# Kernel tuning notes

Measured on AMD Instinct MI355X. Metric: run time of the kernel, lower is better.

The kernel has to match this reference:

```python
import jax, jax.numpy as jnp
import numpy as np

B, C, H, W = 1, 128, 48, 48
HC = 32                     # head_channel
NH = C // HC                # num heads = 4
K = 16                      # n_clusters
N = H * W                   # 2304
SCALE = HC ** 0.5
EPS = 1e-6


def setup_inputs() -> dict:
    key = jax.random.key(0)
    ks = jax.random.split(key, 20)
    s = 0.05  # weight init scale ~ xavier-ish for C=128
    def g(i, shape, sc=s):
        return jax.random.normal(ks[i], shape, dtype=jnp.float32) * sc
    return {
        'q_img': g(0, (B, C, H, W), 1.0),
        'k_img_map': g(1, (B, C, H, W), 1.0),
        'v_img_map': g(2, (B, C, H, W), 1.0),
        'pixel_coefficients': jax.random.uniform(ks[3], (B, N, N), dtype=jnp.float32),
        'labels': jax.random.randint(ks[4], (B, H, W), 0, K),
        # projections (stored as [in, out]; y = x @ w + b)
        'wq': g(5, (C, C)), 'bq': jnp.zeros((C,), jnp.float32),
        'wk': g(6, (C, C)), 'bk': jnp.zeros((C,), jnp.float32),
        'wv': g(7, (C, C)), 'bv': jnp.zeros((C,), jnp.float32),
        # mlp_1: Linear(C,2C) -> LeakyReLU(0.01) -> Linear(2C,C) (dropout=0 -> identity)
        'w1a': g(8, (C, 2 * C)), 'b1a': jnp.zeros((2 * C,), jnp.float32),
        'w1b': g(9, (2 * C, C)), 'b1b': jnp.zeros((C,), jnp.float32),
        # mlp_2
        'w2a': g(10, (C, 2 * C)), 'b2a': jnp.zeros((2 * C,), jnp.float32),
        'w2b': g(11, (2 * C, C)), 'b2b': jnp.zeros((C,), jnp.float32),
    }


def _mlp(x, wa, ba, wb, bb):
    h = x @ wa + ba
    h = jax.nn.leaky_relu(h, negative_slope=0.01)
    return h @ wb + bb


def reference(q_img, k_img_map, v_img_map, pixel_coefficients,
              wq, bq, wk, bk, wv, bv,
              w1a, b1a, w1b, b1b, w2a, b2a, w2b, b2b,
              labels):
    # projections on channel-last pixels
    q = q_img.transpose(0, 2, 3, 1).reshape(B, N, C) @ wq + bq
    k = k_img_map.transpose(0, 2, 3, 1).reshape(B, N, C) @ wk + bk
    v = v_img_map.transpose(0, 2, 3, 1).reshape(B, N, C) @ wv + bv

    labels_flat = labels.reshape(B, N)
    onehot = jax.nn.one_hot(labels_flat, K, dtype=q.dtype)        # [B,N,K]
    num_k = jnp.einsum('bnk,bnc->bkc', onehot, k)                 # [B,K,C]
    den_k = onehot.sum(axis=1)[:, :, None] + EPS                  # [B,K,1]
    centers_k = num_k / den_k

    qm = q.reshape(B, N, NH, HC).transpose(0, 2, 1, 3)            # [B,h,N,d]
    km = k.reshape(B, N, NH, HC).transpose(0, 2, 1, 3)
    vm = v.reshape(B, N, NH, HC).transpose(0, 2, 1, 3)
    kcm = centers_k.reshape(B, K, NH, HC).transpose(0, 2, 1, 3)   # [B,h,K,d]

    attn_intra = jnp.einsum('bhid,bhjd->bhij', qm, km)            # [B,h,N,N]
    attn_centers = jnp.einsum('bhid,bhkd->bhik', qm, kcm)         # [B,h,N,K]

    # gather center score per key's cluster: attn_centers[b,h,i,labels[b,j]]
    idx = jnp.broadcast_to(labels_flat[:, None, None, :], (B, NH, N, N))
    attn_inter = jnp.take_along_axis(attn_centers, idx, axis=3)   # [B,h,N,N]
    attn_inter = attn_inter * pixel_coefficients[:, None, :, :]

    same = labels_flat[:, None, :, None] == labels_flat[:, None, None, :]  # [B,1,N,N]
    scores = jnp.where(same, attn_intra, attn_inter) / SCALE
    attn_w = jax.nn.softmax(scores, axis=-1)

    out = jnp.einsum('bhij,bhjd->bhid', attn_w, vm)
    out = out.transpose(0, 2, 1, 3).reshape(B, N, C)              # [B,N,C]

    v_spatial = v.reshape(B, H, W, C).transpose(0, 3, 1, 2)       # [B,C,H,W]
    rs1 = v_spatial + _mlp(out, w1a, b1a, w1b, b1b).transpose(0, 2, 1).reshape(B, C, H, W)
    rs1_flat = rs1.transpose(0, 2, 3, 1).reshape(B, N, C)
    rs2 = rs1 + _mlp(rs1_flat, w2a, b2a, w2b, b2b).transpose(0, 2, 1).reshape(B, C, H, W)
    return rs2
```

## Files before the change

### kernel.cpp

```cpp
#include <hip/hip_runtime.h>
#include <hip/hip_bf16.h>
#include <math.h>

#define NPIX 2304
#define CCH  128
#define NH   4
#define HC   32
#define NCL  16
#define KSPLIT 8
#define KEYS 288
#define NSTEP 9
#define QSCALE 0.25503489f
#define PPT  16

typedef __attribute__((ext_vector_type(8))) short short8;
typedef __attribute__((ext_vector_type(4))) short short4v;
typedef __attribute__((ext_vector_type(4))) float f32x4;

#if __has_builtin(__builtin_amdgcn_exp2f)
#define EXP2(x) __builtin_amdgcn_exp2f(x)
#else
#define EXP2(x) __expf((x) * 0.6931471805599453f)
#endif

static __device__ __forceinline__ short f2bf(float x) {
    __hip_bfloat16 b = __float2bfloat16(x);
    return *reinterpret_cast<short*>(&b);
}

__global__ void __launch_bounds__(256) proj_kernel(
        const float* __restrict__ xq, const float* __restrict__ xk,
        const float* __restrict__ xv, const int* __restrict__ labels,
        const float* __restrict__ wq, const float* __restrict__ bq,
        const float* __restrict__ wk, const float* __restrict__ bk,
        const float* __restrict__ wv, const float* __restrict__ bv,
        const float* __restrict__ w1a, const float* __restrict__ w1b,
        const float* __restrict__ w2a, const float* __restrict__ w2b,
        short* __restrict__ qbf, short* __restrict__ kbf,
        float* __restrict__ vbuf, short* __restrict__ vbfT,
        float* __restrict__ cpart, float* __restrict__ denpart,
        short* __restrict__ t1a, short* __restrict__ t1b,
        short* __restrict__ t2a, short* __restrict__ t2b) {
    __shared__ float xsP[CCH * PPT];
    __shared__ float ls2[2 * NCL * CCH];
    __shared__ float smls[32];
    const int which = blockIdx.y;
    const int pxblk = blockIdx.x;
    const int t  = threadIdx.x;

    if (which == 3) {
        const int idx = pxblk * 256 + t;
        if (idx < 16384) {
            const int sel = idx >> 12, local = idx & 4095;
            short8 s;
            if (sel == 0 || sel == 2) {
                const float* src = (sel == 0) ? w1a : w2a;
                short*       dst = (sel == 0) ? t1a : t2a;
                const int o = local >> 4, g = local & 15;
#pragma unroll
                for (int j = 0; j < 8; ++j) s[j] = f2bf(src[(g * 8 + j) * 256 + o]);
                *(short8*)(dst + (size_t)o * 128 + g * 8) = s;
            } else {
                const float* src = (sel == 1) ? w1b : w2b;
                short*       dst = (sel == 1) ? t1b : t2b;
                const int o = local >> 5, g = local & 31;
#pragma unroll
                for (int j = 0; j < 8; ++j) s[j] = f2bf(src[(g * 8 + j) * 128 + o]);
                *(short8*)(dst + (size_t)o * 256 + g * 8) = s;
            }
        }
        return;
    }

    const int n0 = pxblk * PPT;
    const int c  = t & 127;
    const int ph = t >> 7;
    const float* x = (which == 0) ? xq : (which == 1) ? xk : xv;
    const float* w = (which == 0) ? wq : (which == 1) ? wk : wv;
    const float* b = (which == 0) ? bq : (which == 1) ? bk : bv;

#pragma unroll
    for (int it = 0; it < 8; ++it) {
        const int flat = it * 256 + t;
        const int cc = flat >> 4;
        const int p  = flat & 15;
        xsP[flat] = x[cc * NPIX + n0 + p];
    }
    if (which == 1)
        for (int u = t; u < 2 * NCL * CCH; u += 256) ls2[u] = 0.f;
    __syncthreads();

    float acc[8];
    const float bb = b[c];
#pragma unroll
    for (int p = 0; p < 8; ++p) acc[p] = bb;

#pragma unroll 4
    for (int in = 0; in < CCH; ++in) {
        const float wv_ = w[in * CCH + c];
        const float4 xa = *(const float4*)(xsP + in * PPT + ph * 8);
        const float4 xb = *(const float4*)(xsP + in * PPT + ph * 8 + 4);
        acc[0] = fmaf(xa.x, wv_, acc[0]); acc[1] = fmaf(xa.y, wv_, acc[1]);
        acc[2] = fmaf(xa.z, wv_, acc[2]); acc[3] = fmaf(xa.w, wv_, acc[3]);
        acc[4] = fmaf(xb.x, wv_, acc[4]); acc[5] = fmaf(xb.y, wv_, acc[5]);
        acc[6] = fmaf(xb.z, wv_, acc[6]); acc[7] = fmaf(xb.w, wv_, acc[7]);
    }

    const int nb = n0 + ph * 8;
    if (which == 0) {
#pragma unroll
        for (int p = 0; p < 8; ++p)
            qbf[(size_t)(nb + p) * CCH + c] = f2bf(acc[p] * QSCALE);
    } else if (which == 1) {
#pragma unroll
        for (int p = 0; p < 8; ++p)
            kbf[(size_t)(nb + p) * CCH + c] = f2bf(acc[p]);
        int lab8[8];
#pragma unroll
        for (int p = 0; p < 8; ++p) lab8[p] = labels[nb + p];
#pragma unroll
        for (int p = 0; p < 8; ++p)
            ls2[(ph * NCL + lab8[p]) * CCH + c] += acc[p];
        if (t < 32) {
            const int g2 = t >> 4, cl = t & 15;
            int cnt = 0;
#pragma unroll
            for (int p = 0; p < 8; ++p)
                cnt += (labels[n0 + g2 * 8 + p] == cl) ? 1 : 0;
            smls[t] = (float)cnt;
        }
        __syncthreads();
        for (int u = t; u < NCL * CCH; u += 256)
            cpart[(size_t)pxblk * 2048 + u] = ls2[u] + ls2[2048 + u];
        if (t < 16)
            denpart[pxblk * 16 + t] = smls[t] + smls[16 + t];
    } else {
#pragma unroll
        for (int p = 0; p < 8; ++p) vbuf[(size_t)(nb + p) * CCH + c] = acc[p];
        short8 s0;
#pragma unroll
        for (int p = 0; p < 8; ++p) s0[p] = f2bf(acc[p]);
        *(short8*)(vbfT + (size_t)c * NPIX + nb) = s0;
    }
}

__global__ void centersB_kernel(const float* __restrict__ cpart,
                                const float* __restrict__ denpart,
                                short* __restrict__ cbf) {
    const int idx = blockIdx.x * 256 + threadIdx.x;
    const int kk  = idx >> 7;
    float den = 0.f, s = 0.f;
    for (int b = 0; b < 144; ++b) den += denpart[b * 16 + kk];
    for (int b = 0; b < 144; ++b) s   += cpart[(size_t)b * 2048 + idx];
    cbf[idx] = f2bf(s / (den + 1e-6f));
}

__global__ void __launch_bounds__(256, 4) attn_part_kernel(
        const short* __restrict__ qbf,  const short* __restrict__ kbf,
        const short* __restrict__ vbfT, const short* __restrict__ cbf,
        const int* __restrict__ labels, const float* __restrict__ pc,
        float* __restrict__ part_o, float* __restrict__ part_l) {
    __shared__ __align__(16) short Pl[NH][16 * 40];
    __shared__ __align__(16) float aclT[NH][16][16];
    __shared__ int   labl[KEYS];
    const int qt   = blockIdx.x;
    const int ks   = blockIdx.y;
    const int tid  = threadIdx.x;
    const int w    = tid >> 6;
    const int lane = tid & 63;
    const int quad = lane >> 4;
    const int lq   = lane & 15;
    const int i0   = qt * 16;
    const int j0   = ks * KEYS;

    for (int u = tid; u < KEYS / 4; u += 256)
        *(int4*)(labl + u * 4) = *(const int4*)(labels + j0 + u * 4);

    const short8 aq = *(const short8*)(qbf + (size_t)(i0 + lq) * CCH + w * HC + quad * 8);
    {
        const short8 bc = *(const short8*)(cbf + (size_t)lq * CCH + w * HC + quad * 8);
        f32x4 z = {0.f, 0.f, 0.f, 0.f};
        f32x4 acd = __builtin_amdgcn_mfma_f32_16x16x32_bf16(aq, bc, z, 0, 0, 0);
        *(f32x4*)(&aclT[w][lq][quad * 4]) = acd;
    }
    int labi[4];
#pragma unroll
    for (int r = 0; r < 4; ++r) labi[r] = labels[i0 + quad * 4 + r];

    __syncthreads();

    const short* kp  = kbf  + (size_t)(j0 + lq) * CCH + w * HC + quad * 8;
    const short* vp  = vbfT + (size_t)(w * HC + lq) * NPIX + j0 + quad * 8;
    const float* pcp = pc   + (size_t)(i0 + quad * 4) * NPIX + j0 + lq;

    short8 k0A, k1A, v0A, v1A, k0B, k1B, v0B, v1B;
    float pcA[8], pcB[8];
    f32x4 accO0 = {0.f, 0.f, 0.f, 0.f};
    f32x4 accO1 = {0.f, 0.f, 0.f, 0.f};
    float lp[4] = {0.f, 0.f, 0.f, 0.f};

#define ISSUE(K0_, K1_, V0_, V1_, s) do {                                         \
        K0_ = *(const short8*)(kp + (size_t)(s) * 32 * CCH);                      \
        K1_ = *(const short8*)(kp + (size_t)((s) * 32 + 16) * CCH);               \
        V0_ = *(const short8*)(vp + (s) * 32);                                    \
        V1_ = *(const short8*)(vp + (size_t)16 * NPIX + (s) * 32);                \
    } while (0)

#define ISSUE_PC(dst, s) do {                                                     \
        _Pragma("unroll")                                                         \
        for (int r_ = 0; r_ < 4; ++r_) {                                          \
            dst[r_ * 2 + 0] = pcp[(size_t)r_ * NPIX + (s) * 32];                  \
            dst[r_ * 2 + 1] = pcp[(size_t)r_ * NPIX + (s) * 32 + 16];             \
        }                                                                         \
    } while (0)

#define COMPUTE(s, K0_, K1_, V0_, V1_, PCUSE) do {                                \
        _Pragma("unroll")                                                         \
        for (int kh = 0; kh < 2; ++kh) {                                          \
            const short8 bk = (kh == 0) ? K0_ : K1_;                              \
            f32x4 z = {0.f, 0.f, 0.f, 0.f};                                       \
            const f32x4 sv = __builtin_amdgcn_mfma_f32_16x16x32_bf16(aq, bk, z, 0, 0, 0);\
            const int slab = labl[(s) * 32 + kh * 16 + lq];                       \
            const f32x4 av4 = *(const f32x4*)(&aclT[w][slab][quad * 4]);          \
            _Pragma("unroll")                                                     \
            for (int r = 0; r < 4; ++r) {                                         \
                const float sc_ = (slab == labi[r]) ? sv[r] : av4[r] * PCUSE[r * 2 + kh];\
                const float p   = EXP2(sc_);                                      \
                lp[r] += p;                                                       \
                Pl[w][(quad * 4 + r) * 40 + kh * 16 + lq] = f2bf(p);              \
            }                                                                     \
        }                                                                         \
        const short8 ap = *(const short8*)(&Pl[w][lq * 40 + quad * 8]);           \
        accO0 = __builtin_amdgcn_mfma_f32_16x16x32_bf16(ap, V0_, accO0, 0, 0, 0); \
        accO1 = __builtin_amdgcn_mfma_f32_16x16x32_bf16(ap, V1_, accO1, 0, 0, 0); \
    } while (0)

    ISSUE(k0A, k1A, v0A, v1A, 0);
    ISSUE_PC(pcA, 0);
    for (int sb = 0; sb < NSTEP; sb += 2) {
        if (sb + 1 < NSTEP) { ISSUE(k0B, k1B, v0B, v1B, sb + 1); ISSUE_PC(pcB, sb + 1); }
        COMPUTE(sb, k0A, k1A, v0A, v1A, pcA);
        if (sb + 1 < NSTEP) {
            if (sb + 2 < NSTEP) { ISSUE(k0A, k1A, v0A, v1A, sb + 2); ISSUE_PC(pcA, sb + 2); }
            COMPUTE(sb + 1, k0B, k1B, v0B, v1B, pcB);
        }
    }
#undef ISSUE
#undef ISSUE_PC
#undef COMPUTE

#pragma unroll
    for (int r = 0; r < 4; ++r) {
        float v = lp[r];
        v += __shfl_xor(v, 1, 64);
        v += __shfl_xor(v, 2, 64);
        v += __shfl_xor(v, 4, 64);
        v += __shfl_xor(v, 8, 64);
        lp[r] = v;
    }
    if (lq == 0) {
#pragma unroll
        for (int r = 0; r < 4; ++r)
            part_l[((size_t)ks * NPIX + i0 + quad * 4 + r) * NH + w] = lp[r];
    }
#pragma unroll
    for (int r = 0; r < 4; ++r) {
        float* po = part_o + ((size_t)ks * NPIX + i0 + quad * 4 + r) * CCH + w * HC;
        po[lq]      = accO0[r];
        po[16 + lq] = accO1[r];
    }
}

#define XS 136
#define HS 264
__global__ void __launch_bounds__(256) mlp_mfma_kernel(
        const float* __restrict__ part_o, const float* __restrict__ part_l,
        const float* __restrict__ vbuf,
        const short* __restrict__ t1a, const float* __restrict__ b1a,
        const short* __restrict__ t1b, const float* __restrict__ b1b,
        const short* __restrict__ t2a, const float* __restrict__ b2a,
        const short* __restrict__ t2b, const float* __restrict__ b2b,
        float* __restrict__ outp) {
    __shared__ __align__(16) short xbf[16 * XS];
    __shared__ __align__(16) short hbf[16 * HS];
    __shared__ __align__(16) short r1bf[16 * XS];
    __shared__ float fT[128 * 20];
    const int n0 = blockIdx.x * 16;
    const int t  = threadIdx.x;
    const int w  = t >> 6, lane = t & 63, quad = lane >> 4, lq = lane & 15;

    for (int u = t; u < 512; u += 256) {
        const int p = u >> 5, c4 = (u & 31) * 4, hh = c4 >> 5;
        float ls_ = 0.f;
#pragma unroll
        for (int ks = 0; ks < KSPLIT; ++ks)
            ls_ += part_l[((size_t)ks * NPIX + n0 + p) * NH + hh];
        float sx = 0.f, sy = 0.f, sz = 0.f, sw2 = 0.f;
#pragma unroll
        for (int ks = 0; ks < KSPLIT; ++ks) {
            const float4 v = *(const float4*)(part_o + ((size_t)ks * NPIX + n0 + p) * CCH + c4);
            sx += v.x; sy += v.y; sz += v.z; sw2 += v.w;
        }
        const float inv = 1.f / ls_;
        short4v s;
        s[0] = f2bf(sx * inv); s[1] = f2bf(sy * inv);
        s[2] = f2bf(sz * inv); s[3] = f2bf(sw2 * inv);
        *(short4v*)(xbf + p * XS + c4) = s;
    }
    __syncthreads();

    {
        short8 a[4];
#pragma unroll
        for (int ks = 0; ks < 4; ++ks)
            a[ks] = *(const short8*)(xbf + lq * XS + ks * 32 + quad * 8);
#pragma unroll
        for (int tile = 0; tile < 4; ++tile) {
            const int out0 = w * 64 + tile * 16;
            f32x4 acc = {0.f, 0.f, 0.f, 0.f};
#pragma unroll
            for (int ks = 0; ks < 4; ++ks) {
                const short8 b = *(const short8*)(t1a + (size_t)(out0 + lq) * 128 + ks * 32 + quad * 8);
                acc = __builtin_amdgcn_mfma_f32_16x16x32_bf16(a[ks], b, acc, 0, 0, 0);
            }
            const float bb = b1a[out0 + lq];
#pragma unroll
            for (int r = 0; r < 4; ++r) {
                float v = acc[r] + bb;
                v = (v > 0.f) ? v : 0.01f * v;
                hbf[(quad * 4 + r) * HS + out0 + lq] = f2bf(v);
            }
        }
    }
    __syncthreads();

    float rs1f[2][4];
    {
        short8 a[8];
#pragma unroll
        for (int ks = 0; ks < 8; ++ks)
            a[ks] = *(const short8*)(hbf + lq * HS + ks * 32 + quad * 8);
#pragma unroll
        for (int tile = 0; tile < 2; ++tile) {
            const int out0 = w * 32 + tile * 16;
            f32x4 acc = {0.f, 0.f, 0.f, 0.f};
#pragma unroll
            for (int ks = 0; ks < 8; ++ks) {
                const short8 b = *(const short8*)(t1b + (size_t)(out0 + lq) * 256 + ks * 32 + quad * 8);
                acc = __builtin_amdgcn_mfma_f32_16x16x32_bf16(a[ks], b, acc, 0, 0, 0);
            }
            const float bb = b1b[out0 + lq];
#pragma unroll
            for (int r = 0; r < 4; ++r) {
                const float v = acc[r] + bb +
                    vbuf[(size_t)(n0 + quad * 4 + r) * CCH + out0 + lq];
                rs1f[tile][r] = v;
                r1bf[(quad * 4 + r) * XS + out0 + lq] = f2bf(v);
            }
        }
    }
    __syncthreads();

    {
        short8 a[4];
#pragma unroll
        for (int ks = 0; ks < 4; ++ks)
            a[ks] = *(const short8*)(r1bf + lq * XS + ks * 32 + quad * 8);
#pragma unroll
        for (int tile = 0; tile < 4; ++tile) {
            const int out0 = w * 64 + tile * 16;
            f32x4 acc = {0.f, 0.f, 0.f, 0.f};
#pragma unroll
            for (int ks = 0; ks < 4; ++ks) {
                const short8 b = *(const short8*)(t2a + (size_t)(out0 + lq) * 128 + ks * 32 + quad * 8);
                acc = __builtin_amdgcn_mfma_f32_16x16x32_bf16(a[ks], b, acc, 0, 0, 0);
            }
            const float bb = b2a[out0 + lq];
#pragma unroll
            for (int r = 0; r < 4; ++r) {
                float v = acc[r] + bb;
                v = (v > 0.f) ? v : 0.01f * v;
                hbf[(quad * 4 + r) * HS + out0 + lq] = f2bf(v);
            }
        }
    }
    __syncthreads();

    {
        short8 a[8];
#pragma unroll
        for (int ks = 0; ks < 8; ++ks)
            a[ks] = *(const short8*)(hbf + lq * HS + ks * 32 + quad * 8);
#pragma unroll
        for (int tile = 0; tile < 2; ++tile) {
            const int out0 = w * 32 + tile * 16;
            f32x4 acc = {0.f, 0.f, 0.f, 0.f};
#pragma unroll
            for (int ks = 0; ks < 8; ++ks) {
                const short8 b = *(const short8*)(t2b + (size_t)(out0 + lq) * 256 + ks * 32 + quad * 8);
                acc = __builtin_amdgcn_mfma_f32_16x16x32_bf16(a[ks], b, acc, 0, 0, 0);
            }
            const float bb = b2b[out0 + lq];
#pragma unroll
            for (int r = 0; r < 4; ++r)
                fT[(out0 + lq) * 20 + quad * 4 + r] = acc[r] + bb + rs1f[tile][r];
        }
    }
    __syncthreads();

    for (int u = t; u < 512; u += 256) {
        const int row = u >> 2, seg = u & 3;
        const float4 v = *(const float4*)(fT + row * 20 + seg * 4);
        *(float4*)(outp + (size_t)row * NPIX + n0 + seg * 4) = v;
    }
}

extern "C" void kernel_launch(void* const* d_in, const int* in_sizes, int n_in,
                              void* d_out, int out_size, void* d_ws, size_t ws_size,
                              hipStream_t stream) {
    const float* q_img = (const float*)d_in[0];
    const float* k_img = (const float*)d_in[1];
    const float* v_img = (const float*)d_in[2];
    const float* pc    = (const float*)d_in[3];
    const int*   labels= (const int*)  d_in[4];
    const float* wq = (const float*)d_in[5];   const float* bq = (const float*)d_in[6];
    const float* wk = (const float*)d_in[7];   const float* bk = (const float*)d_in[8];
    const float* wv = (const float*)d_in[9];   const float* bv = (const float*)d_in[10];
    const float* w1a = (const float*)d_in[11]; const float* b1a = (const float*)d_in[12];
    const float* w1b = (const float*)d_in[13]; const float* b1b = (const float*)d_in[14];
    const float* w2a = (const float*)d_in[15]; const float* b2a = (const float*)d_in[16];
    const float* w2b = (const float*)d_in[17]; const float* b2b = (const float*)d_in[18];

    float* fw = (float*)d_ws;
    float* vbuf    = fw;
    float* part_o  = vbuf + (size_t)NPIX * CCH;
    float* part_l  = part_o + (size_t)KSPLIT * NPIX * CCH;
    float* cpart   = part_l + (size_t)KSPLIT * NPIX * NH;
    float* denpart = cpart + (size_t)144 * 2048;
    short* t1a  = (short*)(denpart + 144 * 16);
    short* t1b  = t1a + 32768;
    short* t2a  = t1b + 32768;
    short* t2b  = t2a + 32768;
    short* qbf  = t2b + 32768;
    short* kbf  = qbf + (size_t)NPIX * CCH;
    short* vbfT = kbf + (size_t)NPIX * CCH;
    short* cbf  = vbfT + (size_t)NPIX * CCH;

    proj_kernel<<<dim3(144, 4), 256, 0, stream>>>(
        q_img, k_img, v_img, labels, wq, bq, wk, bk, wv, bv,
        w1a, w1b, w2a, w2b,
        qbf, kbf, vbuf, vbfT, cpart, denpart, t1a, t1b, t2a, t2b);
    centersB_kernel<<<8, 256, 0, stream>>>(cpart, denpart, cbf);
    attn_part_kernel<<<dim3(144, KSPLIT), 256, 0, stream>>>(
        qbf, kbf, vbfT, cbf, labels, pc, part_o, part_l);
    mlp_mfma_kernel<<<144, 256, 0, stream>>>(
        part_o, part_l, vbuf, t1a, b1a, t1b, b1b, t2a, b2a, t2b, b2b,
        (float*)d_out);
}
```

Before: 159.7 us.

## Compute Q/K/V projections with bf16 MFMA using prepacked transposed weights

```diff
diff --git a/kernel.cpp b/kernel.cpp
--- a/kernel.cpp
+++ b/kernel.cpp
@@ -11,7 +11,6 @@
 #define KEYS 288
 #define NSTEP 9
 #define QSCALE 0.25503489f
-#define PPT  16
 
 typedef __attribute__((ext_vector_type(8))) short short8;
 typedef __attribute__((ext_vector_type(4))) short short4v;
@@ -28,99 +27,128 @@
     return *reinterpret_cast<short*>(&b);
 }
 
+__global__ void __launch_bounds__(256) pack_w_kernel(
+        const float* __restrict__ wq,  const float* __restrict__ wk,
+        const float* __restrict__ wv,
+        const float* __restrict__ w1a, const float* __restrict__ w1b,
+        const float* __restrict__ w2a, const float* __restrict__ w2b,
+        short* __restrict__ tq,  short* __restrict__ tk,
+        short* __restrict__ tv,
+        short* __restrict__ t1a, short* __restrict__ t1b,
+        short* __restrict__ t2a, short* __restrict__ t2b) {
+    const int idx = blockIdx.x * 256 + threadIdx.x;
+    if (idx < 16384) {
+        const int sel = idx >> 12, local = idx & 4095;
+        short8 s;
+        if (sel == 0 || sel == 2) {
+            const float* src = (sel == 0) ? w1a : w2a;
+            short*       dst = (sel == 0) ? t1a : t2a;
+            const int o = local >> 4, g = local & 15;
+#pragma unroll
+            for (int j = 0; j < 8; ++j) s[j] = f2bf(src[(g * 8 + j) * 256 + o]);
+            *(short8*)(dst + (size_t)o * 128 + g * 8) = s;
+        } else {
+            const float* src = (sel == 1) ? w1b : w2b;
+            short*       dst = (sel == 1) ? t1b : t2b;
+            const int o = local >> 5, g = local & 31;
+#pragma unroll
+            for (int j = 0; j < 8; ++j) s[j] = f2bf(src[(g * 8 + j) * 128 + o]);
+            *(short8*)(dst + (size_t)o * 256 + g * 8) = s;
+        }
+    } else if (idx < 22528) {
+        const int i2 = idx - 16384;
+        const int sel = i2 >> 11, local = i2 & 2047;
+        const float* src = (sel == 0) ? wq : (sel == 1) ? wk : wv;
+        short*       dst = (sel == 0) ? tq : (sel == 1) ? tk : tv;
+        const int o = local >> 4, g = local & 15;
+        short8 s;
+#pragma unroll
+        for (int j = 0; j < 8; ++j) s[j] = f2bf(src[(g * 8 + j) * 128 + o]);
+        *(short8*)(dst + (size_t)o * 128 + g * 8) = s;
+    }
+}
+
 __global__ void __launch_bounds__(256) proj_kernel(
         const float* __restrict__ xq, const float* __restrict__ xk,
         const float* __restrict__ xv, const int* __restrict__ labels,
-        const float* __restrict__ wq, const float* __restrict__ bq,
-        const float* __restrict__ wk, const float* __restrict__ bk,
-        const float* __restrict__ wv, const float* __restrict__ bv,
-        const float* __restrict__ w1a, const float* __restrict__ w1b,
-        const float* __restrict__ w2a, const float* __restrict__ w2b,
+        const short* __restrict__ tq, const float* __restrict__ bq,
+        const short* __restrict__ tk, const float* __restrict__ bk,
+        const short* __restrict__ tv, const float* __restrict__ bv,
         short* __restrict__ qbf, short* __restrict__ kbf,
         float* __restrict__ vbuf, short* __restrict__ vbfT,
-        float* __restrict__ cpart, float* __restrict__ denpart,
-        short* __restrict__ t1a, short* __restrict__ t1b,
-        short* __restrict__ t2a, short* __restrict__ t2b) {
-    __shared__ float xsP[CCH * PPT];
+        float* __restrict__ cpart, float* __restrict__ denpart) {
+    __shared__ __align__(16) short xbf[16 * 136];
+    __shared__ float kf[16 * 128];
     __shared__ float ls2[2 * NCL * CCH];
     __shared__ float smls[32];
     const int which = blockIdx.y;
     const int pxblk = blockIdx.x;
     const int t  = threadIdx.x;
 
-    if (which == 3) {
-        const int idx = pxblk * 256 + t;
-        if (idx < 16384) {
-            const int sel = idx >> 12, local = idx & 4095;
-            short8 s;
-            if (sel == 0 || sel == 2) {
-                const float* src = (sel == 0) ? w1a : w2a;
-                short*       dst = (sel == 0) ? t1a : t2a;
-                const int o = local >> 4, g = local & 15;
-#pragma unroll
-                for (int j = 0; j < 8; ++j) s[j] = f2bf(src[(g * 8 + j) * 256 + o]);
-                *(short8*)(dst + (size_t)o * 128 + g * 8) = s;
-            } else {
-                const float* src = (sel == 1) ? w1b : w2b;
-                short*       dst = (sel == 1) ? t1b : t2b;
-                const int o = local >> 5, g = local & 31;
-#pragma unroll
-                for (int j = 0; j < 8; ++j) s[j] = f2bf(src[(g * 8 + j) * 128 + o]);
-                *(short8*)(dst + (size_t)o * 256 + g * 8) = s;
-            }
-        }
-        return;
-    }
-
-    const int n0 = pxblk * PPT;
-    const int c  = t & 127;
-    const int ph = t >> 7;
-    const float* x = (which == 0) ? xq : (which == 1) ? xk : xv;
-    const float* w = (which == 0) ? wq : (which == 1) ? wk : wv;
-    const float* b = (which == 0) ? bq : (which == 1) ? bk : bv;
+    const int n0 = pxblk * 16;
+    const int w    = t >> 6;
+    const int lane = t & 63;
+    const int quad = lane >> 4;
+    const int lq   = lane & 15;
+    const float* x  = (which == 0) ? xq : (which == 1) ? xk : xv;
+    const short* wt = (which == 0) ? tq : (which == 1) ? tk : tv;
+    const float* b  = (which == 0) ? bq : (which == 1) ? bk : bv;
 
 #pragma unroll
     for (int it = 0; it < 8; ++it) {
         const int flat = it * 256 + t;
-        const int cc = flat >> 4;
-        const int p  = flat & 15;
-        xsP[flat] = x[cc * NPIX + n0 + p];
+        const int cc = flat >> 4, p = flat & 15;
+        xbf[p * 136 + cc] = f2bf(x[cc * NPIX + n0 + p]);
     }
     if (which == 1)
         for (int u = t; u < 2 * NCL * CCH; u += 256) ls2[u] = 0.f;
     __syncthreads();
 
-    float acc[8];
-    const float bb = b[c];
-#pragma unroll
-    for (int p = 0; p < 8; ++p) acc[p] = bb;
-
-#pragma unroll 4
-    for (int in = 0; in < CCH; ++in) {
-        const float wv_ = w[in * CCH + c];
-        const float4 xa = *(const float4*)(xsP + in * PPT + ph * 8);
-        const float4 xb = *(const float4*)(xsP + in * PPT + ph * 8 + 4);
-        acc[0] = fmaf(xa.x, wv_, acc[0]); acc[1] = fmaf(xa.y, wv_, acc[1]);
-        acc[2] = fmaf(xa.z, wv_, acc[2]); acc[3] = fmaf(xa.w, wv_, acc[3]);
-        acc[4] = fmaf(xb.x, wv_, acc[4]); acc[5] = fmaf(xb.y, wv_, acc[5]);
-        acc[6] = fmaf(xb.z, wv_, acc[6]); acc[7] = fmaf(xb.w, wv_, acc[7]);
-    }
-
-    const int nb = n0 + ph * 8;
+    short8 a[4];
+#pragma unroll
+    for (int ks = 0; ks < 4; ++ks)
+        a[ks] = *(const short8*)(xbf + lq * 136 + ks * 32 + quad * 8);
+
+    float ov[2][4];
+#pragma unroll
+    for (int tile = 0; tile < 2; ++tile) {
+        const int out0 = w * 32 + tile * 16;
+        f32x4 acc = {0.f, 0.f, 0.f, 0.f};
+#pragma unroll
+        for (int ks = 0; ks < 4; ++ks) {
+            const short8 bw = *(const short8*)(wt + (size_t)(out0 + lq) * 128 + ks * 32 + quad * 8);
+            acc = __builtin_amdgcn_mfma_f32_16x16x32_bf16(a[ks], bw, acc, 0, 0, 0);
+        }
+        const float bb = b[out0 + lq];
+#pragma unroll
+        for (int r = 0; r < 4; ++r) ov[tile][r] = acc[r] + bb;
+    }
+
     if (which == 0) {
 #pragma unroll
+        for (int tile = 0; tile < 2; ++tile)
+#pragma unroll
+            for (int r = 0; r < 4; ++r)
+                qbf[(size_t)(n0 + quad * 4 + r) * CCH + w * 32 + tile * 16 + lq] =
+                    f2bf(ov[tile][r] * QSCALE);
+    } else if (which == 1) {
+#pragma unroll
+        for (int tile = 0; tile < 2; ++tile)
+#pragma unroll
+            for (int r = 0; r < 4; ++r) {
+                const float v = ov[tile][r];
+                const int out0 = w * 32 + tile * 16;
+                kbf[(size_t)(n0 + quad * 4 + r) * CCH + out0 + lq] = f2bf(v);
+                kf[(quad * 4 + r) * 128 + out0 + lq] = v;
+            }
+        __syncthreads();
+        const int c = t & 127, ph = t >> 7;
+        int lab8[8];
+#pragma unroll
+        for (int p = 0; p < 8; ++p) lab8[p] = labels[n0 + ph * 8 + p];
+#pragma unroll
         for (int p = 0; p < 8; ++p)
-            qbf[(size_t)(nb + p) * CCH + c] = f2bf(acc[p] * QSCALE);
-    } else if (which == 1) {
-#pragma unroll
-        for (int p = 0; p < 8; ++p)
-            kbf[(size_t)(nb + p) * CCH + c] = f2bf(acc[p]);
-        int lab8[8];
-#pragma unroll
-        for (int p = 0; p < 8; ++p) lab8[p] = labels[nb + p];
-#pragma unroll
-        for (int p = 0; p < 8; ++p)
-            ls2[(ph * NCL + lab8[p]) * CCH + c] += acc[p];
+            ls2[(ph * NCL + lab8[p]) * CCH + c] += kf[(ph * 8 + p) * 128 + c];
         if (t < 32) {
             const int g2 = t >> 4, cl = t & 15;
             int cnt = 0;
@@ -136,11 +164,14 @@
             denpart[pxblk * 16 + t] = smls[t] + smls[16 + t];
     } else {
 #pragma unroll
-        for (int p = 0; p < 8; ++p) vbuf[(size_t)(nb + p) * CCH + c] = acc[p];
-        short8 s0;
-#pragma unroll
-        for (int p = 0; p < 8; ++p) s0[p] = f2bf(acc[p]);
-        *(short8*)(vbfT + (size_t)c * NPIX + nb) = s0;
+        for (int tile = 0; tile < 2; ++tile)
+#pragma unroll
+            for (int r = 0; r < 4; ++r) {
+                const float v = ov[tile][r];
+                const int out0 = w * 32 + tile * 16;
+                vbuf[(size_t)(n0 + quad * 4 + r) * CCH + out0 + lq] = v;
+                vbfT[(size_t)(out0 + lq) * NPIX + n0 + quad * 4 + r] = f2bf(v);
+            }
     }
 }
 
@@ -441,15 +472,19 @@
     short* t1b  = t1a + 32768;
     short* t2a  = t1b + 32768;
     short* t2b  = t2a + 32768;
-    short* qbf  = t2b + 32768;
+    short* tq   = t2b + 32768;
+    short* tk   = tq + 16384;
+    short* tv   = tk + 16384;
+    short* qbf  = tv + 16384;
     short* kbf  = qbf + (size_t)NPIX * CCH;
     short* vbfT = kbf + (size_t)NPIX * CCH;
     short* cbf  = vbfT + (size_t)NPIX * CCH;
 
-    proj_kernel<<<dim3(144, 4), 256, 0, stream>>>(
-        q_img, k_img, v_img, labels, wq, bq, wk, bk, wv, bv,
-        w1a, w1b, w2a, w2b,
-        qbf, kbf, vbuf, vbfT, cpart, denpart, t1a, t1b, t2a, t2b);
+    pack_w_kernel<<<88, 256, 0, stream>>>(
+        wq, wk, wv, w1a, w1b, w2a, w2b, tq, tk, tv, t1a, t1b, t2a, t2b);
+    proj_kernel<<<dim3(144, 3), 256, 0, stream>>>(
+        q_img, k_img, v_img, labels, tq, bq, tk, bk, tv, bv,
+        qbf, kbf, vbuf, vbfT, cpart, denpart);
     centersB_kernel<<<8, 256, 0, stream>>>(cpart, denpart, cbf);
     attn_part_kernel<<<dim3(144, KSPLIT), 256, 0, stream>>>(
         qbf, kbf, vbfT, cbf, labels, pc, part_o, part_l);
```

After: 155.9 us. 2.3% less time.
